# Optimization experiments

Hardware: AMD Instinct MI355X
Metric: run time of the kernel (lower is better)

The kernel has to match this reference:

```python
import jax, jax.numpy as jnp
import numpy as np

PARENTS = np.array([-1, 0, 1, 1, 1])
NECK_CHAIN = np.array([1, 0])  # neck joint (1) up to root (0)
B, V, F, J, S, E = 512, 5023, 9976, 5, 100, 50
L_STAT, L_DYN, L_FULL, N_BUCKET = 51, 17, 68, 79


def rodrigues(rvec):
    """Axis-angle [N,3] -> rotation matrices [N,3,3]."""
    angle = jnp.linalg.norm(rvec + 1e-8, axis=-1, keepdims=True)  # [N,1]
    axis = rvec / angle
    s = jnp.sin(angle)[..., None]
    c = jnp.cos(angle)[..., None]
    rx, ry, rz = axis[:, 0], axis[:, 1], axis[:, 2]
    z = jnp.zeros_like(rx)
    K = jnp.stack([z, -rz, ry, rz, z, -rx, -ry, rx, z], axis=-1).reshape(-1, 3, 3)
    I = jnp.eye(3, dtype=rvec.dtype)
    return I + s * K + (1.0 - c) * (K @ K)


def verts2lmk(vertices, faces, lmk_faces_idx, lmk_bary):
    lmk_faces = faces[lmk_faces_idx]                               # [B,L,3]
    lmk_verts = jax.vmap(lambda v, f: v[f])(vertices, lmk_faces)   # [B,L,3verts,3xyz]
    return jnp.einsum('blfc,blf->blc', lmk_verts, lmk_bary)


def setup_inputs() -> dict:
    key = jax.random.key(0)
    ks = jax.random.split(key, 16)
    shape_params = jax.random.normal(ks[0], (B, S), jnp.float32)
    expression_params = jax.random.normal(ks[1], (B, E), jnp.float32)
    pose_params = 0.2 * jax.random.normal(ks[2], (B, 6), jnp.float32)
    eye_pose_params = 0.1 * jax.random.normal(ks[3], (B, 6), jnp.float32)
    v_template = jax.random.normal(ks[4], (V, 3), jnp.float32) * 0.1
    shapedirs = jax.random.normal(ks[5], (V, 3, S + E), jnp.float32) * 0.01
    posedirs = jax.random.normal(ks[6], ((J - 1) * 9, V * 3), jnp.float32) * 0.01
    jr = jax.random.uniform(ks[7], (J, V), jnp.float32)
    J_regressor = jr / jnp.sum(jr, axis=1, keepdims=True)
    lbs_weights = jax.nn.softmax(jax.random.normal(ks[8], (V, J), jnp.float32), axis=-1)
    faces = jax.random.randint(ks[9], (F, 3), 0, V)
    lmk_faces_idx = jax.random.randint(ks[10], (L_STAT,), 0, F)
    lb = jax.random.uniform(ks[11], (L_STAT, 3), jnp.float32) + 1e-3
    lmk_bary_coords = lb / jnp.sum(lb, axis=-1, keepdims=True)
    dynamic_lmk_faces_idx = jax.random.randint(ks[12], (N_BUCKET, L_DYN), 0, F)
    db = jax.random.uniform(ks[13], (N_BUCKET, L_DYN, 3), jnp.float32) + 1e-3
    dynamic_lmk_bary_coords = db / jnp.sum(db, axis=-1, keepdims=True)
    full_lmk_faces_idx = jax.random.randint(ks[14], (L_FULL,), 0, F)
    fb = jax.random.uniform(ks[15], (L_FULL, 3), jnp.float32) + 1e-3
    full_lmk_bary_coords = fb / jnp.sum(fb, axis=-1, keepdims=True)
    return {
        'shape_params': shape_params, 'expression_params': expression_params,
        'pose_params': pose_params, 'eye_pose_params': eye_pose_params,
        'v_template': v_template, 'shapedirs': shapedirs, 'posedirs': posedirs,
        'J_regressor': J_regressor, 'lbs_weights': lbs_weights, 'faces': faces,
        'lmk_faces_idx': lmk_faces_idx, 'lmk_bary_coords': lmk_bary_coords,
        'dynamic_lmk_faces_idx': dynamic_lmk_faces_idx,
        'dynamic_lmk_bary_coords': dynamic_lmk_bary_coords,
        'full_lmk_faces_idx': full_lmk_faces_idx,
        'full_lmk_bary_coords': full_lmk_bary_coords,
    }


def reference(shape_params, expression_params, pose_params, eye_pose_params,
              v_template, shapedirs, posedirs, J_regressor, lbs_weights, faces,
              lmk_faces_idx, lmk_bary_coords, dynamic_lmk_faces_idx,
              dynamic_lmk_bary_coords, full_lmk_faces_idx, full_lmk_bary_coords):
    b = shape_params.shape[0]
    nv = v_template.shape[0]
    dt = shape_params.dtype
    betas = jnp.concatenate([shape_params, expression_params], axis=1)          # [B,150]
    neck = jnp.zeros((b, 3), dtype=dt)
    full_pose = jnp.concatenate(
        [pose_params[:, :3], neck, pose_params[:, 3:], eye_pose_params], axis=1)  # [B,15]
    # shape + expression blendshapes
    v_shaped = v_template[None] + jnp.einsum('bl,vcl->bvc', betas, shapedirs)   # [B,V,3]
    joints = jnp.einsum('jv,bvc->bjc', J_regressor, v_shaped)                   # [B,5,3]
    rot_mats = rodrigues(full_pose.reshape(-1, 3)).reshape(b, J, 3, 3)          # [B,5,3,3]
    I3 = jnp.eye(3, dtype=dt)
    pose_feature = (rot_mats[:, 1:] - I3).reshape(b, -1)                        # [B,36]
    v_posed = v_shaped + (pose_feature @ posedirs).reshape(b, nv, 3)
    # kinematic chain -> global joint transforms
    rel_J = joints.at[:, 1:].add(-joints[:, PARENTS[1:]])
    tm = jnp.zeros((b, J, 4, 4), dtype=dt)
    tm = tm.at[:, :, :3, :3].set(rot_mats).at[:, :, :3, 3].set(rel_J).at[:, :, 3, 3].set(1.0)
    chain = [tm[:, 0]]
    for i in range(1, J):
        chain.append(chain[PARENTS[i]] @ tm[:, i])
    A = jnp.stack(chain, axis=1)                                                # [B,5,4,4]
    Rj = jnp.einsum('bjmn,bjn->bjm', A[:, :, :3, :3], joints)
    A_rel = A.at[:, :, :3, 3].add(-Rj)
    # per-vertex skinning
    T = jnp.einsum('vj,bjmn->bvmn', lbs_weights, A_rel)                         # [B,V,4,4]
    vertices = jnp.einsum('bvmn,bvn->bvm', T[:, :, :3, :3], v_posed) + T[:, :, :3, 3]
    # dynamic contour landmark selection from neck kin-chain relative rotation
    aa = full_pose.reshape(b, J, 3)[:, NECK_CHAIN]                              # [B,2,3]
    rc = rodrigues(aa.reshape(-1, 3)).reshape(b, len(NECK_CHAIN), 3, 3)
    rel_rot = jnp.broadcast_to(I3, (b, 3, 3))
    for idx in range(len(NECK_CHAIN)):
        rel_rot = rc[:, idx] @ rel_rot
    sy = jnp.sqrt(rel_rot[:, 0, 0] ** 2 + rel_rot[:, 1, 0] ** 2)
    y_deg = jnp.arctan2(-rel_rot[:, 2, 0], sy) * (180.0 / np.pi)
    y_rot = jnp.round(jnp.minimum(y_deg, 39.0)).astype(jnp.int32)
    neg_mask = y_rot < 0
    big_neg = y_rot < -39
    neg_vals = jnp.where(big_neg, 78, 39 - y_rot)
    y_rot = jnp.where(neg_mask, neg_vals, y_rot)                                # [B] in [0,79)
    dyn_faces = dynamic_lmk_faces_idx[y_rot]                                    # [B,17]
    dyn_bary = dynamic_lmk_bary_coords[y_rot]                                   # [B,17,3]
    lf = jnp.concatenate([dyn_faces, jnp.broadcast_to(lmk_faces_idx[None], (b, lmk_faces_idx.shape[0]))], axis=1)
    lb = jnp.concatenate([dyn_bary, jnp.broadcast_to(lmk_bary_coords[None], (b,) + lmk_bary_coords.shape)], axis=1)
    landmarks2d = verts2lmk(vertices, faces, lf, lb)
    ff = jnp.broadcast_to(full_lmk_faces_idx[None], (b, full_lmk_faces_idx.shape[0]))
    fb = jnp.broadcast_to(full_lmk_bary_coords[None], (b,) + full_lmk_bary_coords.shape)
    landmarks3d = verts2lmk(vertices, faces, ff, fb)
    return (vertices, landmarks2d, landmarks3d)
```

## Files before the change

### kernel.cpp

```cpp
#include <hip/hip_runtime.h>
#include <cstddef>
#include <cstdint>

#define cB   512
#define cV   5023
#define cS   100
#define cE   50
#define cJ   5
#define cLD  17
#define cLF  68

#define cV3    15069
#define cNPAD  15072

#define OUT_V  ((size_t)cB * cV * 3)
#define OUT_L  ((size_t)cB * cLF * 3)

#define WS_PDT    ((size_t)0)
#define WS_ATM    (WS_PDT + 271296)
#define WS_JS2    (WS_ATM + 49152)
#define WS_AREL   (WS_JS2 + 2432)
#define WS_YROT   (WS_AREL + 30720)
#define WS_JSPART (WS_YROT + 512)

typedef __attribute__((ext_vector_type(8))) short short8;
typedef __attribute__((ext_vector_type(4))) float f32x4;

__device__ __forceinline__ unsigned short f2bf(float x) {
  unsigned int u = __float_as_uint(x);
  u = (u + 0x7fffu + ((u >> 16) & 1u)) >> 16;
  return (unsigned short)u;
}

__device__ __forceinline__ void rodrigues9(float rx, float ry, float rz, float* R) {
  float a0 = rx + 1e-8f, a1 = ry + 1e-8f, a2 = rz + 1e-8f;
  float angle = sqrtf(a0 * a0 + a1 * a1 + a2 * a2);
  float inv = 1.0f / angle;
  float x = rx * inv, y = ry * inv, z = rz * inv;
  float s = sinf(angle), c = cosf(angle);
  float t = 1.0f - c;
  float xy = x * y, xz = x * z, yz = y * z;
  R[0] = 1.0f - t * (y * y + z * z);
  R[1] = -s * z + t * xy;
  R[2] =  s * y + t * xz;
  R[3] =  s * z + t * xy;
  R[4] = 1.0f - t * (x * x + z * z);
  R[5] = -s * x + t * yz;
  R[6] = -s * y + t * xz;
  R[7] =  s * x + t * yz;
  R[8] = 1.0f - t * (x * x + y * y);
}

__global__ __launch_bounds__(512) void k_aux(
    const float* __restrict__ sd, const float* __restrict__ pd,
    const float* __restrict__ jreg, const float* __restrict__ vt,
    unsigned int* __restrict__ pdt16_u, float* __restrict__ JSpart) {
  __shared__ unsigned short T[2304];
  const int t = threadIdx.x;
  const int bid = blockIdx.x;
  if (bid < 628) {
    if (t >= 453) return;
    int c = t / 151, l = t - c * 151;
    int v0 = bid * 8;
    float acc[5] = {0.f, 0.f, 0.f, 0.f, 0.f};
#pragma unroll
    for (int vi = 0; vi < 8; ++vi) {
      int v = v0 + vi;
      bool ok = (v < cV);
      int vc = ok ? v : 0;
      float x;
      if (l < 150) x = ok ? sd[(size_t)(v * 3 + c) * 150 + l] : 0.f;
      else         x = ok ? vt[v * 3 + c] : 0.f;
#pragma unroll
      for (int j = 0; j < 5; ++j)
        acc[j] = fmaf(jreg[j * cV + vc], x, acc[j]);
    }
#pragma unroll
    for (int j = 0; j < 5; ++j)
      JSpart[(size_t)bid * 2272 + (j * 3 + c) * 151 + l] = acc[j];
  } else {
    const int n0 = (bid - 628) * 64;
    for (int e = t; e < 2304; e += 512) {
      int kk = e >> 6, ln = e & 63;
      int n = n0 + ln;
      float v = (n < cV3) ? pd[(size_t)kk * cV3 + n] : 0.f;
      T[ln * 36 + kk] = f2bf(v);
    }
    __syncthreads();
    for (int e = t; e < 1152; e += 512) {
      int ln = e / 18, d = e - ln * 18;
      int n = n0 + ln;
      if (n < cNPAD) {
        unsigned int wv = (unsigned int)T[ln * 36 + 2 * d] |
                          ((unsigned int)T[ln * 36 + 2 * d + 1] << 16);
        pdt16_u[(size_t)n * 18 + d] = wv;
      }
    }
  }
}

__global__ __launch_bounds__(256) void k_jsred(const float* __restrict__ JSpart,
                                               float* __restrict__ JS2) {
  __shared__ float red[256];
  const int t = threadIdx.x;
  const int e = blockIdx.x * 32 + (t & 31);
  const int pg = t >> 5;
  float s = 0.f;
  if (e < 2265) {
#pragma unroll 8
    for (int p = pg; p < 628; p += 8)
      s += JSpart[(size_t)p * 2272 + e];
  }
  red[t] = s;
  __syncthreads();
  if (t < 128) red[t] += red[t + 128];
  __syncthreads();
  if (t < 64) red[t] += red[t + 64];
  __syncthreads();
  if (t < 32) {
    float v = red[t] + red[t + 32];
    if (e < 2265) {
      int jc = e / 151, l = e - jc * 151;
      JS2[l * 16 + jc] = v;
    }
  }
}

__global__ __launch_bounds__(256) void k_batch(
    const float* __restrict__ shp, const float* __restrict__ expr,
    const float* __restrict__ pose, const float* __restrict__ eyep,
    const float* __restrict__ JS2g, float* __restrict__ Arel,
    int* __restrict__ yrot, unsigned int* __restrict__ atm_u) {
  __shared__ float js2[151 * 16];
  __shared__ float sb[32 * 153];
  __shared__ float pfs[32 * 36];
  const int t = threadIdx.x;
  const int b0 = blockIdx.x * 32;
  for (int i = t; i < 151 * 16; i += 256) js2[i] = JS2g[i];
  for (int e = t; e < 3200; e += 256) {
    int bl = e / 100, l = e - bl * 100;
    sb[bl * 153 + l] = shp[(size_t)(b0 + bl) * 100 + l];
  }
  for (int e = t; e < 1600; e += 256) {
    int bl = e / 50, l = e - bl * 50;
    sb[bl * 153 + 100 + l] = expr[(size_t)(b0 + bl) * 50 + l];
  }
  __syncthreads();

  if (t < 32) {
    int b = b0 + t;
    float jnt[5][3];
    {
      const f32x4* J4 = (const f32x4*)(js2 + 150 * 16);
      f32x4 A = J4[0], Bq = J4[1], Cq = J4[2], Dq = J4[3];
      jnt[0][0] = A.x;  jnt[0][1] = A.y;  jnt[0][2] = A.z;
      jnt[1][0] = A.w;  jnt[1][1] = Bq.x; jnt[1][2] = Bq.y;
      jnt[2][0] = Bq.z; jnt[2][1] = Bq.w; jnt[2][2] = Cq.x;
      jnt[3][0] = Cq.y; jnt[3][1] = Cq.z; jnt[3][2] = Cq.w;
      jnt[4][0] = Dq.x; jnt[4][1] = Dq.y; jnt[4][2] = Dq.z;
    }
    for (int l = 0; l < 150; ++l) {
      const f32x4* J4 = (const f32x4*)(js2 + l * 16);
      f32x4 A = J4[0], Bq = J4[1], Cq = J4[2], Dq = J4[3];
      float beta = sb[t * 153 + l];
      jnt[0][0] = fmaf(beta, A.x,  jnt[0][0]);
      jnt[0][1] = fmaf(beta, A.y,  jnt[0][1]);
      jnt[0][2] = fmaf(beta, A.z,  jnt[0][2]);
      jnt[1][0] = fmaf(beta, A.w,  jnt[1][0]);
      jnt[1][1] = fmaf(beta, Bq.x, jnt[1][1]);
      jnt[1][2] = fmaf(beta, Bq.y, jnt[1][2]);
      jnt[2][0] = fmaf(beta, Bq.z, jnt[2][0]);
      jnt[2][1] = fmaf(beta, Bq.w, jnt[2][1]);
      jnt[2][2] = fmaf(beta, Cq.x, jnt[2][2]);
      jnt[3][0] = fmaf(beta, Cq.y, jnt[3][0]);
      jnt[3][1] = fmaf(beta, Cq.z, jnt[3][1]);
      jnt[3][2] = fmaf(beta, Cq.w, jnt[3][2]);
      jnt[4][0] = fmaf(beta, Dq.x, jnt[4][0]);
      jnt[4][1] = fmaf(beta, Dq.y, jnt[4][1]);
      jnt[4][2] = fmaf(beta, Dq.z, jnt[4][2]);
    }
    float fp[5][3];
    fp[0][0] = pose[b * 6 + 0]; fp[0][1] = pose[b * 6 + 1]; fp[0][2] = pose[b * 6 + 2];
    fp[1][0] = 0.f; fp[1][1] = 0.f; fp[1][2] = 0.f;
    fp[2][0] = pose[b * 6 + 3]; fp[2][1] = pose[b * 6 + 4]; fp[2][2] = pose[b * 6 + 5];
    fp[3][0] = eyep[b * 6 + 0]; fp[3][1] = eyep[b * 6 + 1]; fp[3][2] = eyep[b * 6 + 2];
    fp[4][0] = eyep[b * 6 + 3]; fp[4][1] = eyep[b * 6 + 4]; fp[4][2] = eyep[b * 6 + 5];
    float R[5][9];
#pragma unroll
    for (int j = 0; j < 5; ++j) rodrigues9(fp[j][0], fp[j][1], fp[j][2], R[j]);
#pragma unroll
    for (int j = 1; j < 5; ++j)
#pragma unroll
      for (int r = 0; r < 9; ++r) {
        float id = (r == 0 || r == 4 || r == 8) ? 1.f : 0.f;
        pfs[t * 36 + (j - 1) * 9 + r] = R[j][r] - id;
      }
    float rel[5][3];
#pragma unroll
    for (int c = 0; c < 3; ++c) {
      rel[0][c] = jnt[0][c];
      rel[1][c] = jnt[1][c] - jnt[0][c];
      rel[2][c] = jnt[2][c] - jnt[1][c];
      rel[3][c] = jnt[3][c] - jnt[1][c];
      rel[4][c] = jnt[4][c] - jnt[1][c];
    }
    float GR[5][9], Gt[5][3];
#pragma unroll
    for (int r = 0; r < 9; ++r) GR[0][r] = R[0][r];
#pragma unroll
    for (int c = 0; c < 3; ++c) Gt[0][c] = rel[0][c];
    const int par[5] = {0, 0, 1, 1, 1};
#pragma unroll
    for (int j = 1; j < 5; ++j) {
      int p = par[j];
#pragma unroll
      for (int r = 0; r < 3; ++r) {
#pragma unroll
        for (int cc = 0; cc < 3; ++cc)
          GR[j][r * 3 + cc] = GR[p][r * 3 + 0] * R[j][0 + cc] +
                              GR[p][r * 3 + 1] * R[j][3 + cc] +
                              GR[p][r * 3 + 2] * R[j][6 + cc];
        Gt[j][r] = Gt[p][r] + GR[p][r * 3 + 0] * rel[j][0] +
                              GR[p][r * 3 + 1] * rel[j][1] +
                              GR[p][r * 3 + 2] * rel[j][2];
      }
    }
#pragma unroll
    for (int j = 0; j < 5; ++j)
#pragma unroll
      for (int r = 0; r < 3; ++r) {
        float tj = Gt[j][r] - (GR[j][r * 3 + 0] * jnt[j][0] +
                               GR[j][r * 3 + 1] * jnt[j][1] +
                               GR[j][r * 3 + 2] * jnt[j][2]);
        Arel[b * 60 + j * 12 + r * 4 + 0] = GR[j][r * 3 + 0];
        Arel[b * 60 + j * 12 + r * 4 + 1] = GR[j][r * 3 + 1];
        Arel[b * 60 + j * 12 + r * 4 + 2] = GR[j][r * 3 + 2];
        Arel[b * 60 + j * 12 + r * 4 + 3] = tj;
      }
    float Ra[9], Rb[9];
    rodrigues9(fp[1][0], fp[1][1], fp[1][2], Ra);
    rodrigues9(fp[0][0], fp[0][1], fp[0][2], Rb);
    float r00 = Rb[0] * Ra[0] + Rb[1] * Ra[3] + Rb[2] * Ra[6];
    float r10 = Rb[3] * Ra[0] + Rb[4] * Ra[3] + Rb[5] * Ra[6];
    float r20 = Rb[6] * Ra[0] + Rb[7] * Ra[3] + Rb[8] * Ra[6];
    float sy = sqrtf(r00 * r00 + r10 * r10);
    float ydeg = atan2f(-r20, sy) * 57.29577951308232f;
    int y = (int)rintf(fminf(ydeg, 39.0f));
    if (y < 0) y = (y < -39) ? 78 : (39 - y);
    yrot[b] = y;
  }
  __syncthreads();

#pragma unroll
  for (int it = 0; it < 12; ++it) {
    int e = t + it * 256;
    int bl = e / 96, d = e - bl * 96;
    unsigned int wv;
    if (d < 75) {
      wv = (unsigned int)f2bf(sb[bl * 153 + 2 * d]) |
           ((unsigned int)f2bf(sb[bl * 153 + 2 * d + 1]) << 16);
    } else if (d < 93) {
      wv = (unsigned int)f2bf(pfs[bl * 36 + (d - 75) * 2]) |
           ((unsigned int)f2bf(pfs[bl * 36 + (d - 75) * 2 + 1]) << 16);
    } else {
      wv = 0u;
    }
    atm_u[(size_t)(b0 + bl) * 96 + d] = wv;
  }
}

__global__ __launch_bounds__(256) void k_main(
    const float* __restrict__ sd, const unsigned int* __restrict__ pdt16_u,
    const unsigned short* __restrict__ ATm, const float* __restrict__ Arel,
    const float* __restrict__ vtempl, const float* __restrict__ lbw,
    float* __restrict__ out) {
  __shared__ __align__(16) unsigned short smem[19200];
  float* Pf = (float*)smem;

  const int bid = blockIdx.x;
  const int r8 = bid & 7, q = bid >> 3;
  const int mb = q & 7, nbh = q >> 3;
  const int nb = (nbh << 3) | r8;
  if (nb >= 157) return;

  const int t = threadIdx.x;
  const int n0 = nb * 96;

  {
    const float* sbase = sd + (size_t)n0 * 150;
    const int vrows = (cV3 - n0 < 96) ? (cV3 - n0) : 96;
    const int vunits = vrows * 75;
#pragma unroll
    for (int it = 0; it < 29; ++it) {
      int u = t + it * 256;
      if (u < 7200) {
        float fx = 0.f, fy = 0.f;
        if (u < vunits) {
          float2 f2 = *(const float2*)(sbase + 2 * (size_t)u);
          fx = f2.x; fy = f2.y;
        }
        unsigned int wv = (unsigned int)f2bf(fx) | ((unsigned int)f2bf(fy) << 16);
        int row = u / 75, cp = u - row * 75;
        *(unsigned int*)((char*)smem + row * 400 + cp * 4) = wv;
      }
    }
    const unsigned int* pdu = pdt16_u + (size_t)n0 * 18;
#pragma unroll
    for (int it = 0; it < 7; ++it) {
      int u = t + it * 256;
      if (u < 1728) {
        unsigned int wv = pdu[u];
        int row = u / 18, d = u - row * 18;
        *(unsigned int*)((char*)smem + row * 400 + 300 + d * 4) = wv;
      }
    }
#pragma unroll
    for (int it = 0; it < 3; ++it) {
      int u = t + it * 256;
      if (u < 672) {
        int row = u / 7, d = u - row * 7;
        *(unsigned int*)((char*)smem + row * 400 + 372 + d * 4) = 0u;
      }
    }
  }
  __syncthreads();

  const int w = t >> 6, L = t & 63;
  const int wm = w >> 1, wn = w & 1;
  const int lr = L & 15, lq = L >> 4;

  f32x4 acc[2][3];
#pragma unroll
  for (int mt = 0; mt < 2; ++mt)
#pragma unroll
    for (int nt = 0; nt < 3; ++nt) acc[mt][nt] = (f32x4){0.f, 0.f, 0.f, 0.f};

  const unsigned short* abase = ATm + ((size_t)mb * 64 + wm * 32 + lr) * 192 + lq * 8;
  short8 af0 = *(const short8*)(abase);
  short8 af1 = *(const short8*)(abase + 16 * 192);
#pragma unroll
  for (int ks = 0; ks < 6; ++ks) {
    short8 nf0, nf1;
    if (ks < 5) {
      nf0 = *(const short8*)(abase + (ks + 1) * 32);
      nf1 = *(const short8*)(abase + 16 * 192 + (ks + 1) * 32);
    }
    const int ko = ks * 32 + lq * 8;
    short8 bf[3];
#pragma unroll
    for (int nt = 0; nt < 3; ++nt)
      bf[nt] = *(const short8*)(smem + (wn * 48 + nt * 16 + lr) * 200 + ko);
#pragma unroll
    for (int nt = 0; nt < 3; ++nt) {
      acc[0][nt] = __builtin_amdgcn_mfma_f32_16x16x32_bf16(af0, bf[nt], acc[0][nt], 0, 0, 0);
      acc[1][nt] = __builtin_amdgcn_mfma_f32_16x16x32_bf16(af1, bf[nt], acc[1][nt], 0, 0, 0);
    }
    af0 = nf0; af1 = nf1;
  }
  __syncthreads();

#pragma unroll
  for (int mt = 0; mt < 2; ++mt)
#pragma unroll
    for (int nt = 0; nt < 3; ++nt) {
      int m_base = wm * 32 + mt * 16 + lq * 4;
      int n_loc  = wn * 48 + nt * 16 + lr;
      *(f32x4*)(Pf + n_loc * 68 + m_base) = acc[mt][nt];
    }
  __syncthreads();

  const int v_loc = t & 31, bgrp = t >> 5;
  const int v = nb * 32 + v_loc;
  float wj[5], vtl[3];
  const bool vok = (v < cV);
#pragma unroll
  for (int j = 0; j < 5; ++j) wj[j] = vok ? lbw[v * 5 + j] : 0.f;
#pragma unroll
  for (int c = 0; c < 3; ++c) vtl[c] = vok ? vtempl[v * 3 + c] : 0.f;

#pragma unroll
  for (int i = 0; i < 8; ++i) {
    const int b_loc = bgrp * 8 + i;
    const float* qb = Arel + ((size_t)mb * 64 + b_loc) * 60;
    float px = Pf[(v_loc * 3 + 0) * 68 + b_loc] + vtl[0];
    float py = Pf[(v_loc * 3 + 1) * 68 + b_loc] + vtl[1];
    float pz = Pf[(v_loc * 3 + 2) * 68 + b_loc] + vtl[2];
    float o0 = 0.f, o1 = 0.f, o2 = 0.f;
#pragma unroll
    for (int j = 0; j < 5; ++j) {
      f32x4 q0 = *(const f32x4*)(qb + j * 12);
      f32x4 q1 = *(const f32x4*)(qb + j * 12 + 4);
      f32x4 q2 = *(const f32x4*)(qb + j * 12 + 8);
      float s0 = q0.x * px + q0.y * py + q0.z * pz + q0.w;
      float s1 = q1.x * px + q1.y * py + q1.z * pz + q1.w;
      float s2 = q2.x * px + q2.y * py + q2.z * pz + q2.w;
      o0 = fmaf(wj[j], s0, o0);
      o1 = fmaf(wj[j], s1, o1);
      o2 = fmaf(wj[j], s2, o2);
    }
    if (vok) {
      const int b = mb * 64 + b_loc;
      size_t off = ((size_t)b * cV + v) * 3;
      out[off + 0] = o0;
      out[off + 1] = o1;
      out[off + 2] = o2;
    }
  }
}

__global__ void k_lmk(const float* __restrict__ verts, const int* __restrict__ faces,
                      const int* __restrict__ lmkf, const float* __restrict__ lmkb,
                      const int* __restrict__ dynf, const float* __restrict__ dynb,
                      const int* __restrict__ fullf, const float* __restrict__ fullb,
                      const int* __restrict__ yrot, float* __restrict__ out) {
  int id = blockIdx.x * 256 + threadIdx.x;
  if (id >= cB * cLF * 2) return;
  int sel = id & 1;
  int r = id >> 1;
  int b = r / cLF, l = r - b * cLF;
  const float* vb = verts + (size_t)b * cV * 3;
  int f; float w0, w1, w2; size_t o;
  if (sel == 0) {
    if (l < cLD) {
      int yb = yrot[b];
      f = dynf[yb * cLD + l];
      const float* bp = dynb + ((size_t)yb * cLD + l) * 3;
      w0 = bp[0]; w1 = bp[1]; w2 = bp[2];
    } else {
      f = lmkf[l - cLD];
      const float* bp = lmkb + (size_t)(l - cLD) * 3;
      w0 = bp[0]; w1 = bp[1]; w2 = bp[2];
    }
    o = OUT_V + ((size_t)b * cLF + l) * 3;
  } else {
    f = fullf[l];
    const float* bp = fullb + (size_t)l * 3;
    w0 = bp[0]; w1 = bp[1]; w2 = bp[2];
    o = OUT_V + OUT_L + ((size_t)b * cLF + l) * 3;
  }
  int i0 = faces[f * 3 + 0] * 3, i1 = faces[f * 3 + 1] * 3, i2 = faces[f * 3 + 2] * 3;
  out[o + 0] = w0 * vb[i0 + 0] + w1 * vb[i1 + 0] + w2 * vb[i2 + 0];
  out[o + 1] = w0 * vb[i0 + 1] + w1 * vb[i1 + 1] + w2 * vb[i2 + 1];
  out[o + 2] = w0 * vb[i0 + 2] + w1 * vb[i1 + 2] + w2 * vb[i2 + 2];
}

extern "C" void kernel_launch(void* const* d_in, const int* in_sizes, int n_in,
                              void* d_out, int out_size, void* d_ws, size_t ws_size,
                              hipStream_t stream) {
  (void)in_sizes; (void)n_in; (void)out_size; (void)ws_size;
  const float* shp  = (const float*)d_in[0];
  const float* expr = (const float*)d_in[1];
  const float* pose = (const float*)d_in[2];
  const float* eyep = (const float*)d_in[3];
  const float* vt   = (const float*)d_in[4];
  const float* sd   = (const float*)d_in[5];
  const float* pd   = (const float*)d_in[6];
  const float* jreg = (const float*)d_in[7];
  const float* lbw  = (const float*)d_in[8];
  const int*   fcs  = (const int*)d_in[9];
  const int*   lmkf = (const int*)d_in[10];
  const float* lmkb = (const float*)d_in[11];
  const int*   dynf = (const int*)d_in[12];
  const float* dynb = (const float*)d_in[13];
  const int*   fullf= (const int*)d_in[14];
  const float* fullb= (const float*)d_in[15];
  float* out = (float*)d_out;
  float* ws  = (float*)d_ws;

  unsigned int*   pdt16 = (unsigned int*)(ws + WS_PDT);
  unsigned short* ATm   = (unsigned short*)(ws + WS_ATM);
  float* JS2    = ws + WS_JS2;
  float* Arel   = ws + WS_AREL;
  int*   yrot   = (int*)(ws + WS_YROT);
  float* JSpart = ws + WS_JSPART;

  k_aux<<<864, 512, 0, stream>>>(sd, pd, jreg, vt, pdt16, JSpart);
  k_jsred<<<71, 256, 0, stream>>>(JSpart, JS2);
  k_batch<<<16, 256, 0, stream>>>(shp, expr, pose, eyep, JS2, Arel, yrot,
                                  (unsigned int*)ATm);
  k_main<<<1280, 256, 0, stream>>>(sd, pdt16, ATm, Arel, vt, lbw, out);
  k_lmk<<<272, 256, 0, stream>>>(out, fcs, lmkf, lmkb, dynf, dynb, fullf, fullb, yrot, out);
}
```

Before: 185.7 us.

## Reuse staged vertex tile across four batch blocks and coalesce output stores

Each k_main block now stages the bf16 shapedirs/posedirs tile once and loops over four 64-batch blocks, instead of one block per (vertex tile, batch block) pair, so the staging conversion is reused. Skinning results go into an LDS output buffer and are written back as contiguous rows, replacing the strided per-vertex xyz stores. Each thread keeps its Arel transforms in registers. The grid shrinks from 1280 to 314 blocks and LDS use rises to 64KB, which lowers occupancy and parallelism in exchange for less redundant global traffic.

```diff
diff --git a/kernel.cpp b/kernel.cpp
--- a/kernel.cpp
+++ b/kernel.cpp
@@ -274,17 +274,33 @@
     const unsigned short* __restrict__ ATm, const float* __restrict__ Arel,
     const float* __restrict__ vtempl, const float* __restrict__ lbw,
     float* __restrict__ out) {
-  __shared__ __align__(16) unsigned short smem[19200];
-  float* Pf = (float*)smem;
+  __shared__ __align__(16) unsigned char smem[64000];
+  unsigned short* Bs = (unsigned short*)smem;
+  float* Pf = (float*)(smem + 38400);
+  float* Ob = (float*)(smem + 51456);
 
   const int bid = blockIdx.x;
-  const int r8 = bid & 7, q = bid >> 3;
-  const int mb = q & 7, nbh = q >> 3;
-  const int nb = (nbh << 3) | r8;
-  if (nb >= 157) return;
-
+  const int nb = bid >> 1, mbh = bid & 1;
   const int t = threadIdx.x;
   const int n0 = nb * 96;
+
+  const int w = t >> 6;
+  const int wm = w >> 1, wn = w & 1;
+  const int L = t & 63, lr = L & 15, lq = L >> 4;
+  const int b_loc = t & 63, vgrp = t >> 6;
+
+  float wjv[2][4][5], vtv[2][4][3];
+#pragma unroll
+  for (int nh = 0; nh < 2; ++nh)
+#pragma unroll
+    for (int i = 0; i < 4; ++i) {
+      int v = nb * 32 + nh * 16 + vgrp * 4 + i;
+      bool ok = (v < cV);
+#pragma unroll
+      for (int j = 0; j < 5; ++j) wjv[nh][i][j] = ok ? lbw[v * 5 + j] : 0.f;
+#pragma unroll
+      for (int c = 0; c < 3; ++c) vtv[nh][i][c] = ok ? vtempl[v * 3 + c] : 0.f;
+    }
 
   {
     const float* sbase = sd + (size_t)n0 * 150;
@@ -301,7 +317,7 @@
         }
         unsigned int wv = (unsigned int)f2bf(fx) | ((unsigned int)f2bf(fy) << 16);
         int row = u / 75, cp = u - row * 75;
-        *(unsigned int*)((char*)smem + row * 400 + cp * 4) = wv;
+        *(unsigned int*)(smem + row * 400 + cp * 4) = wv;
       }
     }
     const unsigned int* pdu = pdt16_u + (size_t)n0 * 18;
@@ -311,7 +327,7 @@
       if (u < 1728) {
         unsigned int wv = pdu[u];
         int row = u / 18, d = u - row * 18;
-        *(unsigned int*)((char*)smem + row * 400 + 300 + d * 4) = wv;
+        *(unsigned int*)(smem + row * 400 + 300 + d * 4) = wv;
       }
     }
 #pragma unroll
@@ -319,91 +335,98 @@
       int u = t + it * 256;
       if (u < 672) {
         int row = u / 7, d = u - row * 7;
-        *(unsigned int*)((char*)smem + row * 400 + 372 + d * 4) = 0u;
+        *(unsigned int*)(smem + row * 400 + 372 + d * 4) = 0u;
       }
     }
   }
   __syncthreads();
 
-  const int w = t >> 6, L = t & 63;
-  const int wm = w >> 1, wn = w & 1;
-  const int lr = L & 15, lq = L >> 4;
-
-  f32x4 acc[2][3];
-#pragma unroll
-  for (int mt = 0; mt < 2; ++mt)
-#pragma unroll
-    for (int nt = 0; nt < 3; ++nt) acc[mt][nt] = (f32x4){0.f, 0.f, 0.f, 0.f};
-
-  const unsigned short* abase = ATm + ((size_t)mb * 64 + wm * 32 + lr) * 192 + lq * 8;
-  short8 af0 = *(const short8*)(abase);
-  short8 af1 = *(const short8*)(abase + 16 * 192);
-#pragma unroll
-  for (int ks = 0; ks < 6; ++ks) {
-    short8 nf0, nf1;
-    if (ks < 5) {
-      nf0 = *(const short8*)(abase + (ks + 1) * 32);
-      nf1 = *(const short8*)(abase + 16 * 192 + (ks + 1) * 32);
-    }
-    const int ko = ks * 32 + lq * 8;
-    short8 bf[3];
-#pragma unroll
-    for (int nt = 0; nt < 3; ++nt)
-      bf[nt] = *(const short8*)(smem + (wn * 48 + nt * 16 + lr) * 200 + ko);
-#pragma unroll
-    for (int nt = 0; nt < 3; ++nt) {
-      acc[0][nt] = __builtin_amdgcn_mfma_f32_16x16x32_bf16(af0, bf[nt], acc[0][nt], 0, 0, 0);
-      acc[1][nt] = __builtin_amdgcn_mfma_f32_16x16x32_bf16(af1, bf[nt], acc[1][nt], 0, 0, 0);
-    }
-    af0 = nf0; af1 = nf1;
-  }
-  __syncthreads();
-
-#pragma unroll
-  for (int mt = 0; mt < 2; ++mt)
-#pragma unroll
-    for (int nt = 0; nt < 3; ++nt) {
-      int m_base = wm * 32 + mt * 16 + lq * 4;
-      int n_loc  = wn * 48 + nt * 16 + lr;
-      *(f32x4*)(Pf + n_loc * 68 + m_base) = acc[mt][nt];
-    }
-  __syncthreads();
-
-  const int v_loc = t & 31, bgrp = t >> 5;
-  const int v = nb * 32 + v_loc;
-  float wj[5], vtl[3];
-  const bool vok = (v < cV);
-#pragma unroll
-  for (int j = 0; j < 5; ++j) wj[j] = vok ? lbw[v * 5 + j] : 0.f;
-#pragma unroll
-  for (int c = 0; c < 3; ++c) vtl[c] = vok ? vtempl[v * 3 + c] : 0.f;
-
-#pragma unroll
-  for (int i = 0; i < 8; ++i) {
-    const int b_loc = bgrp * 8 + i;
+#pragma unroll 1
+  for (int mh = 0; mh < 4; ++mh) {
+    const int mb = mbh * 4 + mh;
+
     const float* qb = Arel + ((size_t)mb * 64 + b_loc) * 60;
-    float px = Pf[(v_loc * 3 + 0) * 68 + b_loc] + vtl[0];
-    float py = Pf[(v_loc * 3 + 1) * 68 + b_loc] + vtl[1];
-    float pz = Pf[(v_loc * 3 + 2) * 68 + b_loc] + vtl[2];
-    float o0 = 0.f, o1 = 0.f, o2 = 0.f;
-#pragma unroll
-    for (int j = 0; j < 5; ++j) {
-      f32x4 q0 = *(const f32x4*)(qb + j * 12);
-      f32x4 q1 = *(const f32x4*)(qb + j * 12 + 4);
-      f32x4 q2 = *(const f32x4*)(qb + j * 12 + 8);
-      float s0 = q0.x * px + q0.y * py + q0.z * pz + q0.w;
-      float s1 = q1.x * px + q1.y * py + q1.z * pz + q1.w;
-      float s2 = q2.x * px + q2.y * py + q2.z * pz + q2.w;
-      o0 = fmaf(wj[j], s0, o0);
-      o1 = fmaf(wj[j], s1, o1);
-      o2 = fmaf(wj[j], s2, o2);
-    }
-    if (vok) {
-      const int b = mb * 64 + b_loc;
-      size_t off = ((size_t)b * cV + v) * 3;
-      out[off + 0] = o0;
-      out[off + 1] = o1;
-      out[off + 2] = o2;
+    f32x4 ar[15];
+#pragma unroll
+    for (int r = 0; r < 15; ++r) ar[r] = *(const f32x4*)(qb + 4 * r);
+
+    f32x4 acc[2][3];
+#pragma unroll
+    for (int mt = 0; mt < 2; ++mt)
+#pragma unroll
+      for (int nt = 0; nt < 3; ++nt) acc[mt][nt] = (f32x4){0.f, 0.f, 0.f, 0.f};
+
+    const unsigned short* abase = ATm + ((size_t)mb * 64 + wm * 32 + lr) * 192 + lq * 8;
+    short8 af0 = *(const short8*)(abase);
+    short8 af1 = *(const short8*)(abase + 16 * 192);
+#pragma unroll
+    for (int ks = 0; ks < 6; ++ks) {
+      short8 nf0, nf1;
+      if (ks < 5) {
+        nf0 = *(const short8*)(abase + (ks + 1) * 32);
+        nf1 = *(const short8*)(abase + 16 * 192 + (ks + 1) * 32);
+      }
+      const int ko = ks * 32 + lq * 8;
+      short8 bf[3];
+#pragma unroll
+      for (int nt = 0; nt < 3; ++nt)
+        bf[nt] = *(const short8*)(Bs + (wn * 48 + nt * 16 + lr) * 200 + ko);
+#pragma unroll
+      for (int nt = 0; nt < 3; ++nt) {
+        acc[0][nt] = __builtin_amdgcn_mfma_f32_16x16x32_bf16(af0, bf[nt], acc[0][nt], 0, 0, 0);
+        acc[1][nt] = __builtin_amdgcn_mfma_f32_16x16x32_bf16(af1, bf[nt], acc[1][nt], 0, 0, 0);
+      }
+      af0 = nf0; af1 = nf1;
+    }
+
+#pragma unroll 1
+    for (int nh = 0; nh < 2; ++nh) {
+      __syncthreads();
+      if (wn == nh) {
+#pragma unroll
+        for (int mt = 0; mt < 2; ++mt)
+#pragma unroll
+          for (int nt = 0; nt < 3; ++nt) {
+            int n_local = nt * 16 + lr;
+            int m = wm * 32 + mt * 16 + lq * 4;
+            *(f32x4*)(Pf + n_local * 68 + m) = acc[mt][nt];
+          }
+      }
+      __syncthreads();
+
+#pragma unroll
+      for (int i = 0; i < 4; ++i) {
+        int vl = vgrp * 4 + i;
+        float px = Pf[(vl * 3 + 0) * 68 + b_loc] + vtv[nh][i][0];
+        float py = Pf[(vl * 3 + 1) * 68 + b_loc] + vtv[nh][i][1];
+        float pz = Pf[(vl * 3 + 2) * 68 + b_loc] + vtv[nh][i][2];
+        float o0 = 0.f, o1 = 0.f, o2 = 0.f;
+#pragma unroll
+        for (int j = 0; j < 5; ++j) {
+          f32x4 q0 = ar[3 * j + 0], q1 = ar[3 * j + 1], q2 = ar[3 * j + 2];
+          float s0 = q0.x * px + q0.y * py + q0.z * pz + q0.w;
+          float s1 = q1.x * px + q1.y * py + q1.z * pz + q1.w;
+          float s2 = q2.x * px + q2.y * py + q2.z * pz + q2.w;
+          float wj = wjv[nh][i][j];
+          o0 = fmaf(wj, s0, o0);
+          o1 = fmaf(wj, s1, o1);
+          o2 = fmaf(wj, s2, o2);
+        }
+        Ob[b_loc * 49 + vl * 3 + 0] = o0;
+        Ob[b_loc * 49 + vl * 3 + 1] = o1;
+        Ob[b_loc * 49 + vl * 3 + 2] = o2;
+      }
+      __syncthreads();
+
+      const int colbase = n0 + nh * 48;
+#pragma unroll
+      for (int it2 = 0; it2 < 12; ++it2) {
+        int idx = t + it2 * 256;
+        int bl = idx / 48, x = idx - bl * 48;
+        int col = colbase + x;
+        if (col < cV3)
+          out[(size_t)(mb * 64 + bl) * cV3 + col] = Ob[bl * 49 + x];
+      }
     }
   }
 }
@@ -478,6 +501,6 @@
   k_jsred<<<71, 256, 0, stream>>>(JSpart, JS2);
   k_batch<<<16, 256, 0, stream>>>(shp, expr, pose, eyep, JS2, Arel, yrot,
                                   (unsigned int*)ATm);
-  k_main<<<1280, 256, 0, stream>>>(sd, pdt16, ATm, Arel, vt, lbw, out);
+  k_main<<<314, 256, 0, stream>>>(sd, pdt16, ATm, Arel, vt, lbw, out);
   k_lmk<<<272, 256, 0, stream>>>(out, fcs, lmkf, lmkb, dynf, dynb, fullf, fullb, yrot, out);
 }
```

Result: slower. 232.1 us (+25.0%).

## Pre-pack combined bf16 B operand in aux kernel; keep Arel in registers in epilogue

Applied to the files above, without the earlier changes.

The aux kernel now builds one padded bf16 B matrix holding the shapedirs and posedirs rows for every n. Previously each of the 8 mb-blocks of k_main re-read and converted fp32 shapedirs itself. k_main now loads its B tile with wide uint4 copies, and lbw and v_template are staged in shared memory. The epilogue is remapped so each thread keeps one batch's Arel transforms in registers, avoiding repeated global loads. The trade-offs are a larger workspace, extra write traffic in k_aux, and higher register pressure in k_main.

```diff
diff --git a/kernel.cpp b/kernel.cpp
--- a/kernel.cpp
+++ b/kernel.cpp
@@ -16,8 +16,8 @@
 #define OUT_V  ((size_t)cB * cV * 3)
 #define OUT_L  ((size_t)cB * cLF * 3)
 
-#define WS_PDT    ((size_t)0)
-#define WS_ATM    (WS_PDT + 271296)
+#define WS_BTN    ((size_t)0)
+#define WS_ATM    (WS_BTN + (size_t)cNPAD * 96)
 #define WS_JS2    (WS_ATM + 49152)
 #define WS_AREL   (WS_JS2 + 2432)
 #define WS_YROT   (WS_AREL + 30720)
@@ -54,8 +54,10 @@
 __global__ __launch_bounds__(512) void k_aux(
     const float* __restrict__ sd, const float* __restrict__ pd,
     const float* __restrict__ jreg, const float* __restrict__ vt,
-    unsigned int* __restrict__ pdt16_u, float* __restrict__ JSpart) {
-  __shared__ unsigned short T[2304];
+    unsigned int* __restrict__ btn_u, float* __restrict__ JSpart) {
+  __shared__ __align__(16) unsigned char sm[44032];
+  float* sdt = (float*)sm;
+  unsigned short* pdt = (unsigned short*)(sm + 38912);
   const int t = threadIdx.x;
   const int bid = blockIdx.x;
   if (bid < 628) {
@@ -80,20 +82,34 @@
       JSpart[(size_t)bid * 2272 + (j * 3 + c) * 151 + l] = acc[j];
   } else {
     const int n0 = (bid - 628) * 64;
+    for (int idx = t; idx < 9600; idx += 512) {
+      size_t g = (size_t)n0 * 150 + idx;
+      float v = (g < (size_t)cV3 * 150) ? sd[g] : 0.f;
+      int row = idx / 150, col = idx - row * 150;
+      sdt[row * 152 + col] = v;
+    }
     for (int e = t; e < 2304; e += 512) {
       int kk = e >> 6, ln = e & 63;
       int n = n0 + ln;
-      float v = (n < cV3) ? pd[(size_t)kk * cV3 + n] : 0.f;
-      T[ln * 36 + kk] = f2bf(v);
+      pdt[ln * 38 + kk] = f2bf((n < cV3) ? pd[(size_t)kk * cV3 + n] : 0.f);
     }
     __syncthreads();
-    for (int e = t; e < 1152; e += 512) {
-      int ln = e / 18, d = e - ln * 18;
-      int n = n0 + ln;
+    for (int e = t; e < 6144; e += 512) {
+      int row = e / 96, d = e - row * 96;
+      int n = n0 + row;
       if (n < cNPAD) {
-        unsigned int wv = (unsigned int)T[ln * 36 + 2 * d] |
-                          ((unsigned int)T[ln * 36 + 2 * d + 1] << 16);
-        pdt16_u[(size_t)n * 18 + d] = wv;
+        unsigned int wv;
+        if (d < 75) {
+          wv = (unsigned int)f2bf(sdt[row * 152 + 2 * d]) |
+               ((unsigned int)f2bf(sdt[row * 152 + 2 * d + 1]) << 16);
+        } else if (d < 93) {
+          int p = (d - 75) * 2;
+          wv = (unsigned int)pdt[row * 38 + p] |
+               ((unsigned int)pdt[row * 38 + p + 1] << 16);
+        } else {
+          wv = 0u;
+        }
+        btn_u[(size_t)n * 96 + d] = wv;
       }
     }
   }
@@ -270,12 +286,14 @@
 }
 
 __global__ __launch_bounds__(256) void k_main(
-    const float* __restrict__ sd, const unsigned int* __restrict__ pdt16_u,
-    const unsigned short* __restrict__ ATm, const float* __restrict__ Arel,
-    const float* __restrict__ vtempl, const float* __restrict__ lbw,
-    float* __restrict__ out) {
-  __shared__ __align__(16) unsigned short smem[19200];
-  float* Pf = (float*)smem;
+    const unsigned short* __restrict__ BTn, const unsigned short* __restrict__ ATm,
+    const float* __restrict__ Arel, const float* __restrict__ vtempl,
+    const float* __restrict__ lbw, float* __restrict__ out) {
+  __shared__ __align__(16) unsigned char smem[39424];
+  unsigned short* Bs = (unsigned short*)smem;
+  float* Pf   = (float*)smem;
+  float* lbwT = (float*)(smem + 38400);
+  float* vtT  = (float*)(smem + 39040);
 
   const int bid = blockIdx.x;
   const int r8 = bid & 7, q = bid >> 3;
@@ -284,50 +302,32 @@
   if (nb >= 157) return;
 
   const int t = threadIdx.x;
-  const int n0 = nb * 96;
-
-  {
-    const float* sbase = sd + (size_t)n0 * 150;
-    const int vrows = (cV3 - n0 < 96) ? (cV3 - n0) : 96;
-    const int vunits = vrows * 75;
-#pragma unroll
-    for (int it = 0; it < 29; ++it) {
-      int u = t + it * 256;
-      if (u < 7200) {
-        float fx = 0.f, fy = 0.f;
-        if (u < vunits) {
-          float2 f2 = *(const float2*)(sbase + 2 * (size_t)u);
-          fx = f2.x; fy = f2.y;
-        }
-        unsigned int wv = (unsigned int)f2bf(fx) | ((unsigned int)f2bf(fy) << 16);
-        int row = u / 75, cp = u - row * 75;
-        *(unsigned int*)((char*)smem + row * 400 + cp * 4) = wv;
-      }
-    }
-    const unsigned int* pdu = pdt16_u + (size_t)n0 * 18;
-#pragma unroll
-    for (int it = 0; it < 7; ++it) {
-      int u = t + it * 256;
-      if (u < 1728) {
-        unsigned int wv = pdu[u];
-        int row = u / 18, d = u - row * 18;
-        *(unsigned int*)((char*)smem + row * 400 + 300 + d * 4) = wv;
-      }
-    }
-#pragma unroll
-    for (int it = 0; it < 3; ++it) {
-      int u = t + it * 256;
-      if (u < 672) {
-        int row = u / 7, d = u - row * 7;
-        *(unsigned int*)((char*)smem + row * 400 + 372 + d * 4) = 0u;
-      }
-    }
-  }
-  __syncthreads();
-
   const int w = t >> 6, L = t & 63;
   const int wm = w >> 1, wn = w & 1;
   const int lr = L & 15, lq = L >> 4;
+
+  const unsigned short* bsrc = BTn + (size_t)nb * 96 * 192;
+  uint4 bst[9];
+#pragma unroll
+  for (int it = 0; it < 9; ++it)
+    bst[it] = *(const uint4*)(bsrc + ((size_t)(t + it * 256)) * 8);
+#pragma unroll
+  for (int it = 0; it < 9; ++it) {
+    int e = t + it * 256;
+    int row = e / 24, col = e - row * 24;
+    *(uint4*)(smem + row * 400 + col * 16) = bst[it];
+  }
+  if (t < 160) {
+    int vl = t / 5, j = t - vl * 5;
+    int v = nb * 32 + vl;
+    lbwT[t] = (v < cV) ? lbw[v * 5 + j] : 0.f;
+  }
+  if (t < 96) {
+    int vl = t / 3, c = t - vl * 3;
+    int v = nb * 32 + vl;
+    vtT[t] = (v < cV) ? vtempl[v * 3 + c] : 0.f;
+  }
+  __syncthreads();
 
   f32x4 acc[2][3];
 #pragma unroll
@@ -349,7 +349,7 @@
     short8 bf[3];
 #pragma unroll
     for (int nt = 0; nt < 3; ++nt)
-      bf[nt] = *(const short8*)(smem + (wn * 48 + nt * 16 + lr) * 200 + ko);
+      bf[nt] = *(const short8*)(Bs + (wn * 48 + nt * 16 + lr) * 200 + ko);
 #pragma unroll
     for (int nt = 0; nt < 3; ++nt) {
       acc[0][nt] = __builtin_amdgcn_mfma_f32_16x16x32_bf16(af0, bf[nt], acc[0][nt], 0, 0, 0);
@@ -357,50 +357,46 @@
     }
     af0 = nf0; af1 = nf1;
   }
+
+  const int b_loc = t >> 2, part = t & 3;
+  const float* qb = Arel + ((size_t)mb * 64 + b_loc) * 60;
+  f32x4 ar[15];
+#pragma unroll
+  for (int r = 0; r < 15; ++r) ar[r] = *(const f32x4*)(qb + 4 * r);
+
   __syncthreads();
 
 #pragma unroll
   for (int mt = 0; mt < 2; ++mt)
 #pragma unroll
     for (int nt = 0; nt < 3; ++nt) {
-      int m_base = wm * 32 + mt * 16 + lq * 4;
-      int n_loc  = wn * 48 + nt * 16 + lr;
-      *(f32x4*)(Pf + n_loc * 68 + m_base) = acc[mt][nt];
-    }
-  __syncthreads();
-
-  const int v_loc = t & 31, bgrp = t >> 5;
-  const int v = nb * 32 + v_loc;
-  float wj[5], vtl[3];
-  const bool vok = (v < cV);
-#pragma unroll
-  for (int j = 0; j < 5; ++j) wj[j] = vok ? lbw[v * 5 + j] : 0.f;
-#pragma unroll
-  for (int c = 0; c < 3; ++c) vtl[c] = vok ? vtempl[v * 3 + c] : 0.f;
+      int n_loc = wn * 48 + nt * 16 + lr;
+      int m = wm * 32 + mt * 16 + lq * 4;
+      *(f32x4*)(Pf + n_loc * 66 + m) = acc[mt][nt];
+    }
+  __syncthreads();
 
 #pragma unroll
   for (int i = 0; i < 8; ++i) {
-    const int b_loc = bgrp * 8 + i;
-    const float* qb = Arel + ((size_t)mb * 64 + b_loc) * 60;
-    float px = Pf[(v_loc * 3 + 0) * 68 + b_loc] + vtl[0];
-    float py = Pf[(v_loc * 3 + 1) * 68 + b_loc] + vtl[1];
-    float pz = Pf[(v_loc * 3 + 2) * 68 + b_loc] + vtl[2];
+    const int vl = part * 8 + i;
+    float px = Pf[(vl * 3 + 0) * 66 + b_loc] + vtT[vl * 3 + 0];
+    float py = Pf[(vl * 3 + 1) * 66 + b_loc] + vtT[vl * 3 + 1];
+    float pz = Pf[(vl * 3 + 2) * 66 + b_loc] + vtT[vl * 3 + 2];
     float o0 = 0.f, o1 = 0.f, o2 = 0.f;
 #pragma unroll
     for (int j = 0; j < 5; ++j) {
-      f32x4 q0 = *(const f32x4*)(qb + j * 12);
-      f32x4 q1 = *(const f32x4*)(qb + j * 12 + 4);
-      f32x4 q2 = *(const f32x4*)(qb + j * 12 + 8);
+      f32x4 q0 = ar[3 * j + 0], q1 = ar[3 * j + 1], q2 = ar[3 * j + 2];
       float s0 = q0.x * px + q0.y * py + q0.z * pz + q0.w;
       float s1 = q1.x * px + q1.y * py + q1.z * pz + q1.w;
       float s2 = q2.x * px + q2.y * py + q2.z * pz + q2.w;
-      o0 = fmaf(wj[j], s0, o0);
-      o1 = fmaf(wj[j], s1, o1);
-      o2 = fmaf(wj[j], s2, o2);
-    }
-    if (vok) {
-      const int b = mb * 64 + b_loc;
-      size_t off = ((size_t)b * cV + v) * 3;
+      float wj = lbwT[vl * 5 + j];
+      o0 = fmaf(wj, s0, o0);
+      o1 = fmaf(wj, s1, o1);
+      o2 = fmaf(wj, s2, o2);
+    }
+    const int v = nb * 32 + vl;
+    if (v < cV) {
+      size_t off = ((size_t)(mb * 64 + b_loc) * cV + v) * 3;
       out[off + 0] = o0;
       out[off + 1] = o1;
       out[off + 2] = o2;
@@ -467,17 +463,17 @@
   float* out = (float*)d_out;
   float* ws  = (float*)d_ws;
 
-  unsigned int*   pdt16 = (unsigned int*)(ws + WS_PDT);
-  unsigned short* ATm   = (unsigned short*)(ws + WS_ATM);
+  unsigned int*   btn  = (unsigned int*)(ws + WS_BTN);
+  unsigned short* ATm  = (unsigned short*)(ws + WS_ATM);
   float* JS2    = ws + WS_JS2;
   float* Arel   = ws + WS_AREL;
   int*   yrot   = (int*)(ws + WS_YROT);
   float* JSpart = ws + WS_JSPART;
 
-  k_aux<<<864, 512, 0, stream>>>(sd, pd, jreg, vt, pdt16, JSpart);
+  k_aux<<<864, 512, 0, stream>>>(sd, pd, jreg, vt, btn, JSpart);
   k_jsred<<<71, 256, 0, stream>>>(JSpart, JS2);
   k_batch<<<16, 256, 0, stream>>>(shp, expr, pose, eyep, JS2, Arel, yrot,
                                   (unsigned int*)ATm);
-  k_main<<<1280, 256, 0, stream>>>(sd, pdt16, ATm, Arel, vt, lbw, out);
+  k_main<<<1280, 256, 0, stream>>>((unsigned short*)btn, ATm, Arel, vt, lbw, out);
   k_lmk<<<272, 256, 0, stream>>>(out, fcs, lmkf, lmkb, dynf, dynb, fullf, fullb, yrot, out);
 }
```

Result: no change. 184.4 us (-0.7%).
